# Kernel tuning notes

Hardware: AMD Instinct MI355X
Metric: run time of the kernel (lower is better)

Reference implementation:

```python
import jax, jax.numpy as jnp
import numpy as np

B, S, D, H = 2, 2048, 1024, 16
DK = D // H

def setup_inputs() -> dict:
    key = jax.random.key(0)
    ks = jax.random.split(key, 9)
    sc = 1.0 / np.sqrt(D)
    return {
        "query": jax.random.normal(ks[0], (B, S, D), jnp.float32),
        "key_": jax.random.normal(ks[1], (B, S, D), jnp.float32),
        "value": jax.random.normal(ks[2], (B, S, D), jnp.float32),
        "Wq": jax.random.normal(ks[3], (D, D), jnp.float32) * sc,
        "bq": jnp.zeros((D,), jnp.float32),
        "Wk": jax.random.normal(ks[4], (D, D), jnp.float32) * sc,
        "bk": jnp.zeros((D,), jnp.float32),
        "Wv": jax.random.normal(ks[5], (D, D), jnp.float32) * sc,
        "bv": jnp.zeros((D,), jnp.float32),
    }

def reference(query, key_, value, Wq, bq, Wk, bk, Wv, bv):
    # QKV projections -> [B, H, S, DK]
    def heads(x, W, b):
        return (x @ W + b).reshape(B, S, H, DK).transpose(0, 2, 1, 3)
    q = heads(query, Wq, bq)
    k = heads(key_, Wk, bk)
    v = heads(value, Wv, bv)
    scores = jnp.einsum('bhsd,bhtd->bhst', q, k) / jnp.sqrt(jnp.float32(DK))
    attn = jax.nn.softmax(scores, axis=-1)  # dropout = identity (eval)
    ctx = jnp.einsum('bhst,bhtd->bhsd', attn, v)
    return ctx.transpose(0, 2, 1, 3).reshape(B, S, D)
```

## Files before the change

kernel.cpp:

```cpp
#include <hip/hip_runtime.h>
#include <hip/hip_bf16.h>

typedef __bf16 bf16x4 __attribute__((ext_vector_type(4)));
typedef __bf16 bf16x8 __attribute__((ext_vector_type(8)));
typedef float  f32x4  __attribute__((ext_vector_type(4)));
typedef float  f32x16 __attribute__((ext_vector_type(16)));

constexpr int B = 2, S = 2048, D = 1024, H = 16, DK = 64;
constexpr int M = B * S;
constexpr int BH = B * H;

__device__ inline float fexp2(float x) {
#if __has_builtin(__builtin_amdgcn_exp2f)
  return __builtin_amdgcn_exp2f(x);
#else
  return exp2f(x);
#endif
}
__device__ inline float frcp(float x) {
#if __has_builtin(__builtin_amdgcn_rcpf)
  return __builtin_amdgcn_rcpf(x);
#else
  return 1.0f / x;
#endif
}
__device__ inline unsigned pk2(float lo, float hi) {
  union { __bf16 h[2]; unsigned u; } x;
  x.h[0] = (__bf16)lo; x.h[1] = (__bf16)hi;
  return x.u;
}

__global__ __launch_bounds__(256) void convx3(const float* __restrict__ x0,
                                              const float* __restrict__ x1,
                                              const float* __restrict__ x2,
                                              __bf16* __restrict__ o0,
                                              __bf16* __restrict__ o1,
                                              __bf16* __restrict__ o2) {
  int z = blockIdx.y;
  const float* in = z == 0 ? x0 : z == 1 ? x1 : x2;
  __bf16* out = z == 0 ? o0 : z == 1 ? o1 : o2;
  int i = (blockIdx.x * 256 + threadIdx.x) * 4;
  float4 v = *(const float4*)(in + i);
  bf16x4 o;
  o[0] = (__bf16)v.x; o[1] = (__bf16)v.y; o[2] = (__bf16)v.z; o[3] = (__bf16)v.w;
  *(bf16x4*)(out + i) = o;
}

__global__ __launch_bounds__(256) void wtrans3(const float* __restrict__ w0,
                                               const float* __restrict__ w1,
                                               const float* __restrict__ w2,
                                               __bf16* __restrict__ t0,
                                               __bf16* __restrict__ t1,
                                               __bf16* __restrict__ t2) {
  int z = blockIdx.z;
  const float* W = z == 0 ? w0 : z == 1 ? w1 : w2;
  __bf16* WT = z == 0 ? t0 : z == 1 ? t1 : t2;
  __shared__ float t[32][33];
  int tx = threadIdx.x & 31, ty0 = threadIdx.x >> 5;
  int n0 = blockIdx.x * 32, k0 = blockIdx.y * 32;
#pragma unroll
  for (int i = 0; i < 4; ++i)
    t[ty0 + i * 8][tx] = W[(size_t)(k0 + ty0 + i * 8) * D + n0 + tx];
  __syncthreads();
#pragma unroll
  for (int i = 0; i < 4; ++i)
    WT[(size_t)(n0 + ty0 + i * 8) * D + k0 + tx] = (__bf16)t[tx][ty0 + i * 8];
}

constexpr int TM = 128, TN = 128, BK = 32;

__global__ __launch_bounds__(256) void proj3(
    const __bf16* __restrict__ X0, const __bf16* __restrict__ X1,
    const __bf16* __restrict__ X2, const __bf16* __restrict__ W0,
    const __bf16* __restrict__ W1, const __bf16* __restrict__ W2,
    const float* __restrict__ b0, const float* __restrict__ b1,
    const float* __restrict__ b2, __bf16* __restrict__ Qo,
    __bf16* __restrict__ Ko, __bf16* __restrict__ Vo) {
  __shared__ __align__(16) __bf16 As[TM * BK];
  __shared__ __align__(16) __bf16 Bs[TN * BK];
  int z = blockIdx.z;
  const __bf16* A  = z == 0 ? X0 : z == 1 ? X1 : X2;
  const __bf16* BT = z == 0 ? W0 : z == 1 ? W1 : W2;
  const float* bias = z == 0 ? b0 : z == 1 ? b1 : b2;
  __bf16* out = z == 0 ? Qo : z == 1 ? Ko : Vo;
  int mode = (z == 2) ? 1 : 0;
  float osc = (z == 0) ? 0.18033688011112042f : 1.0f;

  int t = threadIdx.x;
  int m0 = blockIdx.y * TM, n0 = blockIdx.x * TN;
  int w = t >> 6, lane = t & 63, c = lane & 15, g = lane >> 4;
  int wr = w >> 1, wc = w & 1;

  f32x4 acc[4][4];
#pragma unroll
  for (int i = 0; i < 4; ++i)
#pragma unroll
    for (int j = 0; j < 4; ++j) acc[i][j] = f32x4{0.f, 0.f, 0.f, 0.f};

  int srow = t >> 2;
  int scol = (t & 3) * 8;
  const __bf16* ag = A + (size_t)(m0 + srow) * D + scol;
  const __bf16* bg = BT + (size_t)(n0 + srow) * D + scol;

  for (int kk = 0; kk < D; kk += BK) {
    __builtin_amdgcn_global_load_lds(
        (const __attribute__((address_space(1))) unsigned int*)(ag + kk),
        (__attribute__((address_space(3))) unsigned int*)(As + t * 8), 16, 0, 0);
    __builtin_amdgcn_global_load_lds(
        (const __attribute__((address_space(1))) unsigned int*)(ag + (size_t)64 * D + kk),
        (__attribute__((address_space(3))) unsigned int*)(As + 2048 + t * 8), 16, 0, 0);
    __builtin_amdgcn_global_load_lds(
        (const __attribute__((address_space(1))) unsigned int*)(bg + kk),
        (__attribute__((address_space(3))) unsigned int*)(Bs + t * 8), 16, 0, 0);
    __builtin_amdgcn_global_load_lds(
        (const __attribute__((address_space(1))) unsigned int*)(bg + (size_t)64 * D + kk),
        (__attribute__((address_space(3))) unsigned int*)(Bs + 2048 + t * 8), 16, 0, 0);
    __syncthreads();

    bf16x8 af[4], bf[4];
#pragma unroll
    for (int i = 0; i < 4; ++i)
      af[i] = *(const bf16x8*)(As + (wr * 64 + i * 16 + c) * 32 + g * 8);
#pragma unroll
    for (int j = 0; j < 4; ++j)
      bf[j] = *(const bf16x8*)(Bs + (wc * 64 + j * 16 + c) * 32 + g * 8);
#pragma unroll
    for (int i = 0; i < 4; ++i)
#pragma unroll
      for (int j = 0; j < 4; ++j)
        acc[i][j] = __builtin_amdgcn_mfma_f32_16x16x32_bf16(af[i], bf[j], acc[i][j], 0, 0, 0);
    __syncthreads();
  }

#pragma unroll
  for (int i = 0; i < 4; ++i)
#pragma unroll
    for (int j = 0; j < 4; ++j) {
      int n = n0 + wc * 64 + j * 16 + c;
      float bv = bias[n];
      int h = n >> 6, dk = n & 63;
#pragma unroll
      for (int q = 0; q < 4; ++q) {
        int mrow = m0 + wr * 64 + i * 16 + g * 4 + q;
        int b = mrow >> 11, s = mrow & (S - 1);
        float val = (acc[i][j][q] + bv) * osc;
        size_t idx;
        if (mode == 0) idx = ((size_t)(b * H + h) * S + s) * DK + dk;
        else           idx = ((size_t)(b * H + h) * DK + dk) * S + s;
        out[idx] = (__bf16)val;
      }
    }
}

constexpr int NSTEP = S / 128;

__global__ __launch_bounds__(256) void attn(const __bf16* __restrict__ Q,
                                            const __bf16* __restrict__ K,
                                            const __bf16* __restrict__ VT,
                                            float* __restrict__ out) {
  __shared__ __align__(16) __bf16 Ks[2][8192];
  __shared__ __align__(16) __bf16 Vs[2][8192];

  int t = threadIdx.x, w = t >> 6, lane = t & 63;
  int l31 = lane & 31, hi = lane >> 5;

  int fid = blockIdx.x;
  int xcd = fid & 7, slot = fid >> 3;
  int bh = xcd * 4 + (slot >> 4);
  int q0 = (slot & 15) * 128 + w * 32;

  const __bf16* Qb = Q + (size_t)bh * S * DK;
  const char* Kg = (const char*)(K + (size_t)bh * S * DK);
  const char* Vg = (const char*)(VT + (size_t)bh * DK * S);

  bf16x8 qf[4];
  {
    const __bf16* qp = Qb + (size_t)(q0 + l31) * DK + hi * 8;
#pragma unroll
    for (int s2 = 0; s2 < 4; ++s2) qf[s2] = *(const bf16x8*)(qp + s2 * 16);
  }

  f32x16 acc0, acc1;
#pragma unroll
  for (int r = 0; r < 16; ++r) { acc0[r] = 0.f; acc1[r] = 0.f; }
  float lrun = 0.f;

  int krow = ((l31 >> 2) & 1) * 8 + ((l31 >> 3) & 1) * 16 + ((l31 >> 4) & 1) * 4 + (l31 & 3);
  int kswz = (((krow & 7) ^ ((krow >> 3) & 3)) << 4);
  int vswz = (((l31 & 7) ^ ((l31 >> 3) & 3)) << 4);

  auto stage = [&](int bufi, int kstep) {
#pragma unroll
    for (int i = 0; i < 4; ++i) {
      int L = i * 4096 + t * 16;
      {
        int row = L >> 7;
        int sz = (((row & 7) ^ ((row >> 3) & 3)) << 4);
        __builtin_amdgcn_global_load_lds(
            (const __attribute__((address_space(1))) unsigned int*)(Kg + (size_t)kstep * 16384 + (L ^ sz)),
            (__attribute__((address_space(3))) unsigned int*)((char*)&Ks[bufi][0] + L), 16, 0, 0);
      }
      {
        int row = L >> 8;
        int sz = (((row & 7) ^ ((row >> 3) & 3)) << 4);
        __builtin_amdgcn_global_load_lds(
            (const __attribute__((address_space(1))) unsigned int*)(Vg + (size_t)row * (S * 2) + kstep * 256 + ((L & 255) ^ sz)),
            (__attribute__((address_space(3))) unsigned int*)((char*)&Vs[bufi][0] + L), 16, 0, 0);
      }
    }
  };

  stage(0, 0);
  __syncthreads();

  for (int tt = 0; tt < NSTEP; ++tt) {
    int cur = tt & 1;
    if (tt + 1 < NSTEP) stage(cur ^ 1, tt + 1);
    const char* kb = (const char*)&Ks[cur][0];
    const char* vb = (const char*)&Vs[cur][0];

#pragma unroll
    for (int sub = 0; sub < 4; ++sub) {
      bf16x8 Kf[4], Vf[4];
      {
        const char* kr = kb + ((sub * 32 + krow) << 7);
#pragma unroll
        for (int s2 = 0; s2 < 4; ++s2)
          Kf[s2] = *(const bf16x8*)(kr + ((s2 * 32 + hi * 16) ^ kswz));
      }
#pragma unroll
      for (int ks = 0; ks < 2; ++ks)
#pragma unroll
        for (int db = 0; db < 2; ++db)
          Vf[ks * 2 + db] = *(const bf16x8*)(vb + ((db * 32 + l31) << 8) +
                                             ((sub * 64 + ks * 32 + hi * 16) ^ vswz));

      f32x16 st;
#pragma unroll
      for (int r = 0; r < 16; ++r) st[r] = 0.f;
#pragma unroll
      for (int s2 = 0; s2 < 4; ++s2)
        st = __builtin_amdgcn_mfma_f32_32x32x16_bf16(Kf[s2], qf[s2], st, 0, 0, 0);

      float p[16];
#pragma unroll
      for (int r = 0; r < 16; ++r) p[r] = fexp2(st[r]);
      {
        float t0 = (p[0] + p[1]) + (p[2] + p[3]);
        float t1 = (p[4] + p[5]) + (p[6] + p[7]);
        float t2 = (p[8] + p[9]) + (p[10] + p[11]);
        float t3 = (p[12] + p[13]) + (p[14] + p[15]);
        lrun += (t0 + t1) + (t2 + t3);
      }

      union Pk { unsigned u[4]; bf16x8 v; } P0, P1;
      P0.u[0] = pk2(p[0], p[1]);   P0.u[1] = pk2(p[2], p[3]);
      P0.u[2] = pk2(p[8], p[9]);   P0.u[3] = pk2(p[10], p[11]);
      P1.u[0] = pk2(p[4], p[5]);   P1.u[1] = pk2(p[6], p[7]);
      P1.u[2] = pk2(p[12], p[13]); P1.u[3] = pk2(p[14], p[15]);

      acc0 = __builtin_amdgcn_mfma_f32_32x32x16_bf16(P0.v, Vf[0], acc0, 0, 0, 0);
      acc1 = __builtin_amdgcn_mfma_f32_32x32x16_bf16(P0.v, Vf[1], acc1, 0, 0, 0);
      acc0 = __builtin_amdgcn_mfma_f32_32x32x16_bf16(P1.v, Vf[2], acc0, 0, 0, 0);
      acc1 = __builtin_amdgcn_mfma_f32_32x32x16_bf16(P1.v, Vf[3], acc1, 0, 0, 0);
    }
    __syncthreads();
  }

  lrun += __shfl_xor(lrun, 32);
  int b = bh >> 4, h = bh & 15;
#pragma unroll
  for (int r = 0; r < 16; ++r) {
    int rowq = (r & 3) + 8 * (r >> 2) + 4 * hi;
    float li = __shfl(lrun, rowq);
    float ri = frcp(li);
    size_t base = (size_t)(b * S + q0 + rowq) * D + h * 64 + l31;
    out[base] = acc0[r] * ri;
    out[base + 32] = acc1[r] * ri;
  }
}

extern "C" void kernel_launch(void* const* d_in, const int* in_sizes, int n_in,
                              void* d_out, int out_size, void* d_ws, size_t ws_size,
                              hipStream_t stream) {
  (void)in_sizes; (void)n_in; (void)out_size; (void)ws_size;
  const float* xq = (const float*)d_in[0];
  const float* xk = (const float*)d_in[1];
  const float* xv = (const float*)d_in[2];
  const float* Wq = (const float*)d_in[3];
  const float* bq = (const float*)d_in[4];
  const float* Wk = (const float*)d_in[5];
  const float* bk = (const float*)d_in[6];
  const float* Wv = (const float*)d_in[7];
  const float* bv = (const float*)d_in[8];

  char* ws = (char*)d_ws;
  const size_t MB = 1u << 20;
  __bf16* Xc[3] = {(__bf16*)(ws + 0 * MB), (__bf16*)(ws + 8 * MB), (__bf16*)(ws + 16 * MB)};
  __bf16* WT[3] = {(__bf16*)(ws + 24 * MB), (__bf16*)(ws + 26 * MB), (__bf16*)(ws + 28 * MB)};
  __bf16* Qb = (__bf16*)(ws + 30 * MB);
  __bf16* Kb = (__bf16*)(ws + 38 * MB);
  __bf16* Vt = (__bf16*)(ws + 46 * MB);

  convx3<<<dim3((M * D) / (4 * 256), 3), 256, 0, stream>>>(xq, xk, xv, Xc[0], Xc[1], Xc[2]);
  wtrans3<<<dim3(D / 32, D / 32, 3), 256, 0, stream>>>(Wq, Wk, Wv, WT[0], WT[1], WT[2]);
  proj3<<<dim3(D / TN, M / TM, 3), 256, 0, stream>>>(Xc[0], Xc[1], Xc[2],
                                                     WT[0], WT[1], WT[2],
                                                     bq, bk, bv, Qb, Kb, Vt);
  attn<<<dim3(512), 256, 0, stream>>>(Qb, Kb, Vt, (float*)d_out);
}
```

Before: 113.4 us.

## Fuse fp32-to-bf16 input conversion into projection GEMM with register prefetch and XCD-aware tiling

Drops the separate convx3 kernel. The projection GEMM now reads fp32 activations directly, converts them to bf16 in registers and stores them to LDS, prefetching the next K-slice into registers while the MFMAs run. It also remaps the block index so neighbouring tiles land on the same XCD for L2 reuse, and sets a min-blocks-per-CU launch bound. This removes one kernel launch plus the write and re-read of the bf16 activation buffers. In exchange it reads fp32 (twice the bytes) on every N-tile pass, replaces the async global-to-LDS loads with synchronous register staging, and adds register pressure.

```diff
diff --git a/kernel.cpp b/kernel.cpp
--- a/kernel.cpp
+++ b/kernel.cpp
@@ -28,22 +28,6 @@
   union { __bf16 h[2]; unsigned u; } x;
   x.h[0] = (__bf16)lo; x.h[1] = (__bf16)hi;
   return x.u;
-}
-
-__global__ __launch_bounds__(256) void convx3(const float* __restrict__ x0,
-                                              const float* __restrict__ x1,
-                                              const float* __restrict__ x2,
-                                              __bf16* __restrict__ o0,
-                                              __bf16* __restrict__ o1,
-                                              __bf16* __restrict__ o2) {
-  int z = blockIdx.y;
-  const float* in = z == 0 ? x0 : z == 1 ? x1 : x2;
-  __bf16* out = z == 0 ? o0 : z == 1 ? o1 : o2;
-  int i = (blockIdx.x * 256 + threadIdx.x) * 4;
-  float4 v = *(const float4*)(in + i);
-  bf16x4 o;
-  o[0] = (__bf16)v.x; o[1] = (__bf16)v.y; o[2] = (__bf16)v.z; o[3] = (__bf16)v.w;
-  *(bf16x4*)(out + i) = o;
 }
 
 __global__ __launch_bounds__(256) void wtrans3(const float* __restrict__ w0,
@@ -69,9 +53,9 @@
 
 constexpr int TM = 128, TN = 128, BK = 32;
 
-__global__ __launch_bounds__(256) void proj3(
-    const __bf16* __restrict__ X0, const __bf16* __restrict__ X1,
-    const __bf16* __restrict__ X2, const __bf16* __restrict__ W0,
+__global__ __launch_bounds__(256, 3) void proj3(
+    const float* __restrict__ X0, const float* __restrict__ X1,
+    const float* __restrict__ X2, const __bf16* __restrict__ W0,
     const __bf16* __restrict__ W1, const __bf16* __restrict__ W2,
     const float* __restrict__ b0, const float* __restrict__ b1,
     const float* __restrict__ b2, __bf16* __restrict__ Qo,
@@ -79,7 +63,7 @@
   __shared__ __align__(16) __bf16 As[TM * BK];
   __shared__ __align__(16) __bf16 Bs[TN * BK];
   int z = blockIdx.z;
-  const __bf16* A  = z == 0 ? X0 : z == 1 ? X1 : X2;
+  const float* A   = z == 0 ? X0 : z == 1 ? X1 : X2;
   const __bf16* BT = z == 0 ? W0 : z == 1 ? W1 : W2;
   const float* bias = z == 0 ? b0 : z == 1 ? b1 : b2;
   __bf16* out = z == 0 ? Qo : z == 1 ? Ko : Vo;
@@ -87,7 +71,10 @@
   float osc = (z == 0) ? 0.18033688011112042f : 1.0f;
 
   int t = threadIdx.x;
-  int m0 = blockIdx.y * TM, n0 = blockIdx.x * TN;
+  int fid = blockIdx.x;
+  int xcd = fid & 7, slot = fid >> 3;
+  int m0 = (xcd * 4 + (slot >> 3)) * TM;
+  int n0 = (slot & 7) * TN;
   int w = t >> 6, lane = t & 63, c = lane & 15, g = lane >> 4;
   int wr = w >> 1, wc = w & 1;
 
@@ -99,16 +86,23 @@
 
   int srow = t >> 2;
   int scol = (t & 3) * 8;
-  const __bf16* ag = A + (size_t)(m0 + srow) * D + scol;
+  const float* ag = A + (size_t)(m0 + srow) * D + scol;
+  const float* ag2 = ag + (size_t)64 * D;
   const __bf16* bg = BT + (size_t)(n0 + srow) * D + scol;
 
+  float4 na0 = *(const float4*)(ag + 0);
+  float4 na1 = *(const float4*)(ag + 4);
+  float4 na2 = *(const float4*)(ag2 + 0);
+  float4 na3 = *(const float4*)(ag2 + 4);
+
   for (int kk = 0; kk < D; kk += BK) {
-    __builtin_amdgcn_global_load_lds(
-        (const __attribute__((address_space(1))) unsigned int*)(ag + kk),
-        (__attribute__((address_space(3))) unsigned int*)(As + t * 8), 16, 0, 0);
-    __builtin_amdgcn_global_load_lds(
-        (const __attribute__((address_space(1))) unsigned int*)(ag + (size_t)64 * D + kk),
-        (__attribute__((address_space(3))) unsigned int*)(As + 2048 + t * 8), 16, 0, 0);
+    bf16x8 wa, wb;
+    wa[0] = (__bf16)na0.x; wa[1] = (__bf16)na0.y; wa[2] = (__bf16)na0.z; wa[3] = (__bf16)na0.w;
+    wa[4] = (__bf16)na1.x; wa[5] = (__bf16)na1.y; wa[6] = (__bf16)na1.z; wa[7] = (__bf16)na1.w;
+    wb[0] = (__bf16)na2.x; wb[1] = (__bf16)na2.y; wb[2] = (__bf16)na2.z; wb[3] = (__bf16)na2.w;
+    wb[4] = (__bf16)na3.x; wb[5] = (__bf16)na3.y; wb[6] = (__bf16)na3.z; wb[7] = (__bf16)na3.w;
+    *(bf16x8*)(As + t * 8) = wa;
+    *(bf16x8*)(As + 2048 + t * 8) = wb;
     __builtin_amdgcn_global_load_lds(
         (const __attribute__((address_space(1))) unsigned int*)(bg + kk),
         (__attribute__((address_space(3))) unsigned int*)(Bs + t * 8), 16, 0, 0);
@@ -116,6 +110,13 @@
         (const __attribute__((address_space(1))) unsigned int*)(bg + (size_t)64 * D + kk),
         (__attribute__((address_space(3))) unsigned int*)(Bs + 2048 + t * 8), 16, 0, 0);
     __syncthreads();
+
+    if (kk + BK < D) {
+      na0 = *(const float4*)(ag + kk + BK);
+      na1 = *(const float4*)(ag + kk + BK + 4);
+      na2 = *(const float4*)(ag2 + kk + BK);
+      na3 = *(const float4*)(ag2 + kk + BK + 4);
+    }
 
     bf16x8 af[4], bf[4];
 #pragma unroll
@@ -296,16 +297,14 @@
 
   char* ws = (char*)d_ws;
   const size_t MB = 1u << 20;
-  __bf16* Xc[3] = {(__bf16*)(ws + 0 * MB), (__bf16*)(ws + 8 * MB), (__bf16*)(ws + 16 * MB)};
   __bf16* WT[3] = {(__bf16*)(ws + 24 * MB), (__bf16*)(ws + 26 * MB), (__bf16*)(ws + 28 * MB)};
   __bf16* Qb = (__bf16*)(ws + 30 * MB);
   __bf16* Kb = (__bf16*)(ws + 38 * MB);
   __bf16* Vt = (__bf16*)(ws + 46 * MB);
 
-  convx3<<<dim3((M * D) / (4 * 256), 3), 256, 0, stream>>>(xq, xk, xv, Xc[0], Xc[1], Xc[2]);
   wtrans3<<<dim3(D / 32, D / 32, 3), 256, 0, stream>>>(Wq, Wk, Wv, WT[0], WT[1], WT[2]);
-  proj3<<<dim3(D / TN, M / TM, 3), 256, 0, stream>>>(Xc[0], Xc[1], Xc[2],
-                                                     WT[0], WT[1], WT[2],
-                                                     bq, bk, bv, Qb, Kb, Vt);
+  proj3<<<dim3(256, 1, 3), 256, 0, stream>>>(xq, xk, xv,
+                                             WT[0], WT[1], WT[2],
+                                             bq, bk, bv, Qb, Kb, Vt);
   attn<<<dim3(512), 256, 0, stream>>>(Qb, Kb, Vt, (float*)d_out);
 }
```

Result: faster. 105.6 us (-6.9%).
